# Kernel optimization log

Measured on AMD Instinct MI355X. Metric: run time of the kernel, lower is better.

## Reference

```python
import jax, jax.numpy as jnp
import numpy as np

MEM = 128   # mem_dim
K = 4096    # number of object keys (each an array leaf list)
L = 128     # numbers per array
STATS_CAP = 100  # number_stats list capped at 100 entries


def setup_inputs() -> dict:
    key = jax.random.key(0)
    ks = jax.random.split(key, 13)
    s = 0.05
    return {
        "numbers": jax.random.normal(ks[0], (K, L), jnp.float32),
        "w_num": jax.random.normal(ks[1], (MEM,), jnp.float32) * s,
        "b_num": jax.random.normal(ks[2], (MEM,), jnp.float32) * s,
        "W_ih": jax.random.normal(ks[3], (4 * MEM, 2 * MEM), jnp.float32) * s,
        "W_hh": jax.random.normal(ks[4], (4 * MEM, MEM), jnp.float32) * s,
        "b_ih": jax.random.normal(ks[5], (4 * MEM,), jnp.float32) * s,
        "b_hh": jax.random.normal(ks[6], (4 * MEM,), jnp.float32) * s,
        "W_fh": jax.random.normal(ks[7], (MEM, MEM), jnp.float32) * s,
        "b_fh": jax.random.normal(ks[8], (MEM,), jnp.float32) * s,
        "W_iouh": jax.random.normal(ks[9], (3 * MEM, MEM), jnp.float32) * s,
        "b_iouh": jax.random.normal(ks[10], (3 * MEM,), jnp.float32) * s,
        "W_lout": jax.random.normal(ks[11], (MEM, MEM), jnp.float32) * s,
        "b_lout": jax.random.normal(ks[12], (MEM,), jnp.float32) * s,
    }


def _normalize_numbers(x_flat):
    # Replicates embed_number's running number_stats (tie_primitives -> one shared
    # '___default___' stats list, filled in traversal order, capped at 100 entries).
    # The k-th number is normalized by mean/std over the first min(k, 100) numbers
    # (including itself); std division only when len > 3 and std not ~0.
    n = x_flat.shape[0]
    k = jnp.arange(1, n + 1, dtype=jnp.float32)
    cs = jnp.cumsum(x_flat)
    css = jnp.cumsum(x_flat * x_flat)
    cap = jnp.minimum(k, float(STATS_CAP))
    cs_c = jnp.where(k <= STATS_CAP, cs, cs[STATS_CAP - 1])
    css_c = jnp.where(k <= STATS_CAP, css, css[STATS_CAP - 1])
    mean = cs_c / cap
    var = jnp.maximum(css_c / cap - mean * mean, 0.0)
    std = jnp.sqrt(var)
    # torch impl computes stats with numpy -> no gradient flows through them
    mean = jax.lax.stop_gradient(mean)
    std = jax.lax.stop_gradient(std)
    y = x_flat - mean
    use_std = (cap > 3.0) & (std > 1e-8)
    return jnp.where(use_std, y / jnp.where(use_std, std, 1.0), y)


def _forward(numbers, w_num, b_num, W_ih, W_hh, b_ih, b_hh,
             W_fh, b_fh, W_iouh, b_iouh, W_lout, b_lout):
    # --- embed_number: per-leaf (c=0, h = Linear(1, MEM)(norm_num)) ---
    x = _normalize_numbers(numbers.reshape(-1)).reshape(K, L)
    h_num = x[..., None] * w_num + b_num  # [K, L, MEM]

    # --- embed_array: LSTMCell over each array's children; input = cat([c_child, h_child]) ---
    # child_c is always 0 for number leaves.
    def step(carry, h_t):  # h_t: [K, MEM]
        c, h = carry
        xcat = jnp.concatenate([jnp.zeros_like(h_t), h_t], axis=-1)  # [K, 2*MEM]
        gates = xcat @ W_ih.T + b_ih + h @ W_hh.T + b_hh             # [K, 4*MEM]
        i, f, g, o = jnp.split(gates, 4, axis=-1)
        c2 = jax.nn.sigmoid(f) * c + jax.nn.sigmoid(i) * jnp.tanh(g)
        h2 = jax.nn.sigmoid(o) * jnp.tanh(c2)
        return (c2, h2), None

    z = jnp.zeros((K, MEM), numbers.dtype)
    (c_arr, h_arr), _ = jax.lax.scan(step, (z, z), jnp.swapaxes(h_num, 0, 1))
    # c_arr, h_arr: [K, MEM] final states per array child of the root object

    # --- embed_object (root): child-sum Tree-LSTM gating ---
    f_g = jax.nn.sigmoid(h_arr @ W_fh.T + b_fh)             # [K, MEM]
    fc_sum = jnp.sum(f_g * c_arr, axis=0, keepdims=True)    # [1, MEM]
    hs_bar = jnp.sum(h_arr, axis=0, keepdims=True)          # [1, MEM]
    iou = hs_bar @ W_iouh.T + b_iouh
    i, o, u = jnp.split(iou, 3, axis=-1)
    c = jax.nn.sigmoid(i) * jnp.tanh(u) + fc_sum
    h = jax.nn.sigmoid(o) * jnp.tanh(c)
    h_hat = h @ W_lout.T + b_lout
    return jnp.concatenate([c, h_hat], axis=1)  # [1, 2*MEM]


def reference(numbers, w_num, b_num, W_ih, W_hh, b_ih, b_hh,
              W_fh, b_fh, W_iouh, b_iouh, W_lout, b_lout):
    return _forward(numbers, w_num, b_num, W_ih, W_hh, b_ih, b_hh,
                    W_fh, b_fh, W_iouh, b_iouh, W_lout, b_lout)
```

## Files before the change

kernel.cpp:

```cpp
#include <hip/hip_runtime.h>
#include <math.h>

#define MEM 128
#define HSTR 136

typedef __bf16 bf16x8 __attribute__((ext_vector_type(8)));
typedef float  f32x4  __attribute__((ext_vector_type(4)));

__device__ __forceinline__ float fast_rcp(float x) { return __builtin_amdgcn_rcpf(x); }
__device__ __forceinline__ float fast_sigmoid(float x) {
    return fast_rcp(1.0f + __expf(-x));
}
__device__ __forceinline__ float fast_tanh(float x) {
    return 1.0f - 2.0f * fast_rcp(__expf(2.0f * x) + 1.0f);
}

__global__ void prep_kernel(const float* __restrict__ numbers,
                            const float* __restrict__ w_num,
                            const float* __restrict__ b_num,
                            const float* __restrict__ W_ih,
                            const float* __restrict__ b_ih,
                            const float* __restrict__ b_hh,
                            float* __restrict__ mean_lut, float* __restrict__ inv_lut,
                            float* __restrict__ Avec, float* __restrict__ Bvec) {
    __shared__ float sx[100];
    int tid = threadIdx.x;
    if (tid < 100) sx[tid] = numbers[tid];
    __syncthreads();
    if (tid < 100) {
        float s = 0.f, ss = 0.f;
        for (int j = 0; j <= tid; ++j) { float v = sx[j]; s += v; ss += v * v; }
        float cap  = (float)(tid + 1);
        float mean = s / cap;
        float var  = ss / cap - mean * mean;
        if (var < 0.f) var = 0.f;
        float sd = sqrtf(var);
        float inv = (cap > 3.0f && sd > 1e-8f) ? (1.0f / sd) : 1.0f;
        mean_lut[tid] = mean;
        inv_lut[tid]  = inv;
    }
    if (tid < 512) {
        const float* row = W_ih + tid * 256 + 128;
        float a = 0.f, b = 0.f;
        #pragma unroll 8
        for (int m = 0; m < 128; ++m) { a += row[m] * w_num[m]; b += row[m] * b_num[m]; }
        Avec[tid] = a;
        Bvec[tid] = b + b_ih[tid] + b_hh[tid];
    }
}

__global__ __launch_bounds__(512, 2) void lstm_kernel(
        const float* __restrict__ numbers, const float* __restrict__ W_hh,
        const float* __restrict__ W_fh,    const float* __restrict__ b_fh,
        const float* __restrict__ mean_lut, const float* __restrict__ inv_lut,
        const float* __restrict__ Avec,     const float* __restrict__ Bvec,
        float* __restrict__ fc_sum, float* __restrict__ hs_bar) {
    __shared__ unsigned short hbuf[2][16 * HSTR];
    __shared__ float xls[128 * 16];

    const int tid  = threadIdx.x;
    const int lane = tid & 63;
    const int wave = tid >> 6;
    const int quad = lane >> 4;
    const int lcol = lane & 15;
    const int m0   = wave * 16;
    const int r0   = blockIdx.x * 16;

    for (int i = tid; i < 16 * 128; i += 512) {
        int row = i >> 7;
        int t   = i & 127;
        int flat = (r0 + row) * 128 + t;
        int ii = (flat < 100) ? flat : 99;
        float v = numbers[flat];
        xls[t * 16 + row] = (v - mean_lut[ii]) * inv_lut[ii];
    }
    for (int i = tid; i < 16 * HSTR; i += 512) hbuf[0][i] = 0;

    bf16x8 bf[4][4];
    #pragma unroll
    for (int g = 0; g < 4; ++g) {
        #pragma unroll
        for (int kk = 0; kk < 4; ++kk) {
            int j = g * 128 + m0 + lcol;
            const float* p = W_hh + j * 128 + kk * 32 + quad * 8;
            f32x4 w0 = *(const f32x4*)p;
            f32x4 w1 = *(const f32x4*)(p + 4);
            bf16x8 bt;
            #pragma unroll
            for (int q = 0; q < 4; ++q) { bt[q] = (__bf16)w0[q]; bt[q + 4] = (__bf16)w1[q]; }
            bf[g][kk] = bt;
        }
    }
    float ag[4], bg[4];
    #pragma unroll
    for (int g = 0; g < 4; ++g) {
        ag[g] = Avec[g * 128 + m0 + lcol];
        bg[g] = Bvec[g * 128 + m0 + lcol];
    }

    float c[4]  = {0.f, 0.f, 0.f, 0.f};
    float hf[4] = {0.f, 0.f, 0.f, 0.f};
    __syncthreads();

    auto step = [&](int t, const unsigned short* hin, unsigned short* hout) {
        bf16x8 af[4];
        #pragma unroll
        for (int kk = 0; kk < 4; ++kk)
            af[kk] = *(const bf16x8*)(const void*)(hin + lcol * HSTR + kk * 32 + quad * 8);
        f32x4 xq = *(const f32x4*)(const void*)(xls + t * 16 + quad * 4);
        f32x4 acc[4];
        #pragma unroll
        for (int g = 0; g < 4; ++g) {
            f32x4 a0;
            #pragma unroll
            for (int r = 0; r < 4; ++r) a0[r] = xq[r] * ag[g] + bg[g];
            #pragma unroll
            for (int kk = 0; kk < 4; ++kk)
                a0 = __builtin_amdgcn_mfma_f32_16x16x32_bf16(af[kk], bf[g][kk], a0, 0, 0, 0);
            acc[g] = a0;
        }
        #pragma unroll
        for (int r = 0; r < 4; ++r) {
            float si = fast_sigmoid(acc[0][r]);
            float sf = fast_sigmoid(acc[1][r]);
            float tg = fast_tanh(acc[2][r]);
            float so = fast_sigmoid(acc[3][r]);
            float c2 = sf * c[r] + si * tg;
            c[r] = c2;
            float h = so * fast_tanh(c2);
            hf[r] = h;
            hout[(quad * 4 + r) * HSTR + m0 + lcol] = __builtin_bit_cast(unsigned short, (__bf16)h);
        }
        __syncthreads();
    };

    for (int t = 0; t < 128; t += 2) {
        step(t,     hbuf[0], hbuf[1]);
        step(t + 1, hbuf[1], hbuf[0]);
    }

    float v = hf[0] + hf[1] + hf[2] + hf[3];
    v += __shfl_xor(v, 16);
    v += __shfl_xor(v, 32);
    if (lane < 16) atomicAdd(&hs_bar[m0 + lane], v);

    f32x4 facc;
    {
        float bb = b_fh[m0 + lcol];
        #pragma unroll
        for (int r = 0; r < 4; ++r) facc[r] = bb;
    }
    #pragma unroll
    for (int kk = 0; kk < 4; ++kk) {
        bf16x8 afr = *(const bf16x8*)(const void*)(hbuf[0] + lcol * HSTR + kk * 32 + quad * 8);
        const float* p = W_fh + (m0 + lcol) * 128 + kk * 32 + quad * 8;
        f32x4 w0 = *(const f32x4*)p;
        f32x4 w1 = *(const f32x4*)(p + 4);
        bf16x8 wt;
        #pragma unroll
        for (int q = 0; q < 4; ++q) { wt[q] = (__bf16)w0[q]; wt[q + 4] = (__bf16)w1[q]; }
        facc = __builtin_amdgcn_mfma_f32_16x16x32_bf16(afr, wt, facc, 0, 0, 0);
    }
    float fcv = 0.f;
    #pragma unroll
    for (int r = 0; r < 4; ++r) fcv += fast_sigmoid(facc[r]) * c[r];
    fcv += __shfl_xor(fcv, 16);
    fcv += __shfl_xor(fcv, 32);
    if (lane < 16) atomicAdd(&fc_sum[m0 + lane], fcv);
}

__global__ void finalize_kernel(const float* __restrict__ fc_sum,
                                const float* __restrict__ hs_bar,
                                const float* __restrict__ W_iouh,
                                const float* __restrict__ b_iouh,
                                const float* __restrict__ W_lout,
                                const float* __restrict__ b_lout,
                                float* __restrict__ out) {
    __shared__ float hsb[128], iou[384], hfin[128];
    int tid = threadIdx.x;
    if (tid < 128) hsb[tid] = hs_bar[tid];
    __syncthreads();
    if (tid < 384) {
        float s = b_iouh[tid];
        const float* row = W_iouh + tid * 128;
        #pragma unroll 8
        for (int m = 0; m < 128; ++m) s += row[m] * hsb[m];
        iou[tid] = s;
    }
    __syncthreads();
    if (tid < 128) {
        float i = iou[tid], o = iou[128 + tid], u = iou[256 + tid];
        float cf = fast_sigmoid(i) * fast_tanh(u) + fc_sum[tid];
        out[tid] = cf;
        hfin[tid] = fast_sigmoid(o) * fast_tanh(cf);
    }
    __syncthreads();
    if (tid < 128) {
        float s = b_lout[tid];
        const float* row = W_lout + tid * 128;
        #pragma unroll 8
        for (int k = 0; k < 128; ++k) s += row[k] * hfin[k];
        out[128 + tid] = s;
    }
}

extern "C" void kernel_launch(void* const* d_in, const int* in_sizes, int n_in,
                              void* d_out, int out_size, void* d_ws, size_t ws_size,
                              hipStream_t stream) {
    const float* numbers = (const float*)d_in[0];
    const float* w_num   = (const float*)d_in[1];
    const float* b_num   = (const float*)d_in[2];
    const float* W_ih    = (const float*)d_in[3];
    const float* W_hh    = (const float*)d_in[4];
    const float* b_ih    = (const float*)d_in[5];
    const float* b_hh    = (const float*)d_in[6];
    const float* W_fh    = (const float*)d_in[7];
    const float* b_fh    = (const float*)d_in[8];
    const float* W_iouh  = (const float*)d_in[9];
    const float* b_iouh  = (const float*)d_in[10];
    const float* W_lout  = (const float*)d_in[11];
    const float* b_lout  = (const float*)d_in[12];
    float* out = (float*)d_out;

    float* ws       = (float*)d_ws;
    float* fc_sum   = ws;
    float* hs_bar   = ws + 128;
    float* mean_lut = ws + 256;
    float* inv_lut  = ws + 356;
    float* Avec     = ws + 456;
    float* Bvec     = ws + 968;

    hipMemsetAsync(fc_sum, 0, 256 * sizeof(float), stream);
    prep_kernel<<<1, 512, 0, stream>>>(numbers, w_num, b_num, W_ih, b_ih, b_hh,
                                       mean_lut, inv_lut, Avec, Bvec);
    lstm_kernel<<<256, 512, 0, stream>>>(numbers, W_hh, W_fh, b_fh,
                                         mean_lut, inv_lut, Avec, Bvec, fc_sum, hs_bar);
    finalize_kernel<<<1, 384, 0, stream>>>(fc_sum, hs_bar, W_iouh, b_iouh, W_lout, b_lout, out);
}
```

Before: 218.5 us.

## Split LSTM gates across two wave groups and fold log2e scaling into weights

The LSTM kernel now runs 1024 threads per block. Waves 0-7 compute the input and cell-candidate gates and pass their product through shared memory. Waves 8-15 compute the forget and output gates, update c and h, and write h. The log2(e) factors are folded into W_hh, Avec/Bvec and W_fh so activations become a single exp2 plus reciprocal. The prep kernel is spread over 65 blocks with a wave reduction and now also zeroes the accumulators, which removes the memset. The finalize kernel uses vector loads. The split adds a second barrier per timestep and a shared-memory exchange, in return for halving the MFMA and transcendental work per wave on the serial recurrence path.

```diff
diff --git a/kernel.cpp b/kernel.cpp
--- a/kernel.cpp
+++ b/kernel.cpp
@@ -1,18 +1,15 @@
 #include <hip/hip_runtime.h>
 #include <math.h>
 
-#define MEM 128
+#define L2E 1.4426950408889634f
 #define HSTR 136
+#define PRS 16
 
 typedef __bf16 bf16x8 __attribute__((ext_vector_type(8)));
 typedef float  f32x4  __attribute__((ext_vector_type(4)));
 
-__device__ __forceinline__ float fast_rcp(float x) { return __builtin_amdgcn_rcpf(x); }
-__device__ __forceinline__ float fast_sigmoid(float x) {
-    return fast_rcp(1.0f + __expf(-x));
-}
-__device__ __forceinline__ float fast_tanh(float x) {
-    return 1.0f - 2.0f * fast_rcp(__expf(2.0f * x) + 1.0f);
+__device__ __forceinline__ float sig2(float y) {
+    return __builtin_amdgcn_rcpf(1.0f + __builtin_amdgcn_exp2f(-y));
 }
 
 __global__ void prep_kernel(const float* __restrict__ numbers,
@@ -21,35 +18,52 @@
                             const float* __restrict__ W_ih,
                             const float* __restrict__ b_ih,
                             const float* __restrict__ b_hh,
-                            float* __restrict__ mean_lut, float* __restrict__ inv_lut,
-                            float* __restrict__ Avec, float* __restrict__ Bvec) {
-    __shared__ float sx[100];
-    int tid = threadIdx.x;
-    if (tid < 100) sx[tid] = numbers[tid];
-    __syncthreads();
-    if (tid < 100) {
-        float s = 0.f, ss = 0.f;
-        for (int j = 0; j <= tid; ++j) { float v = sx[j]; s += v; ss += v * v; }
-        float cap  = (float)(tid + 1);
-        float mean = s / cap;
-        float var  = ss / cap - mean * mean;
-        if (var < 0.f) var = 0.f;
-        float sd = sqrtf(var);
-        float inv = (cap > 3.0f && sd > 1e-8f) ? (1.0f / sd) : 1.0f;
-        mean_lut[tid] = mean;
-        inv_lut[tid]  = inv;
-    }
-    if (tid < 512) {
-        const float* row = W_ih + tid * 256 + 128;
-        float a = 0.f, b = 0.f;
-        #pragma unroll 8
-        for (int m = 0; m < 128; ++m) { a += row[m] * w_num[m]; b += row[m] * b_num[m]; }
-        Avec[tid] = a;
-        Bvec[tid] = b + b_ih[tid] + b_hh[tid];
-    }
-}
-
-__global__ __launch_bounds__(512, 2) void lstm_kernel(
+                            float* __restrict__ ws_base) {
+    float* fc_hs    = ws_base;
+    float* mean_lut = ws_base + 256;
+    float* inv_lut  = ws_base + 356;
+    float* Avec     = ws_base + 456;
+    float* Bvec     = ws_base + 968;
+
+    if (blockIdx.x == 64) {
+        __shared__ float sx[100];
+        int tid = threadIdx.x;
+        if (tid < 256) fc_hs[tid] = 0.0f;
+        if (tid < 100) sx[tid] = numbers[tid];
+        __syncthreads();
+        if (tid < 100) {
+            float s = 0.f, ss = 0.f;
+            for (int j = 0; j <= tid; ++j) { float v = sx[j]; s += v; ss += v * v; }
+            float cap  = (float)(tid + 1);
+            float mean = s / cap;
+            float var  = ss / cap - mean * mean;
+            if (var < 0.f) var = 0.f;
+            float sd = sqrtf(var);
+            float inv = (cap > 3.0f && sd > 1e-8f) ? (1.0f / sd) : 1.0f;
+            mean_lut[tid] = mean;
+            inv_lut[tid]  = inv;
+        }
+        return;
+    }
+    int j    = blockIdx.x * 8 + (threadIdx.x >> 6);
+    int lane = threadIdx.x & 63;
+    const float* row = W_ih + j * 256 + 128;
+    float r1 = row[lane], r2 = row[lane + 64];
+    float a = r1 * w_num[lane] + r2 * w_num[lane + 64];
+    float b = r1 * b_num[lane] + r2 * b_num[lane + 64];
+    #pragma unroll
+    for (int off = 32; off >= 1; off >>= 1) {
+        a += __shfl_xor(a, off);
+        b += __shfl_xor(b, off);
+    }
+    if (lane == 0) {
+        float s = (j >= 256 && j < 384) ? (2.0f * L2E) : L2E;
+        Avec[j] = a * s;
+        Bvec[j] = (b + b_ih[j] + b_hh[j]) * s;
+    }
+}
+
+__global__ __launch_bounds__(1024, 4) void lstm_kernel(
         const float* __restrict__ numbers, const float* __restrict__ W_hh,
         const float* __restrict__ W_fh,    const float* __restrict__ b_fh,
         const float* __restrict__ mean_lut, const float* __restrict__ inv_lut,
@@ -57,16 +71,18 @@
         float* __restrict__ fc_sum, float* __restrict__ hs_bar) {
     __shared__ unsigned short hbuf[2][16 * HSTR];
     __shared__ float xls[128 * 16];
+    __shared__ float pbuf[128 * PRS];
 
     const int tid  = threadIdx.x;
     const int lane = tid & 63;
     const int wave = tid >> 6;
+    const bool low = wave < 8;
     const int quad = lane >> 4;
     const int lcol = lane & 15;
-    const int m0   = wave * 16;
+    const int m0   = (wave & 7) * 16;
     const int r0   = blockIdx.x * 16;
 
-    for (int i = tid; i < 16 * 128; i += 512) {
+    for (int i = tid; i < 16 * 128; i += 1024) {
         int row = i >> 7;
         int t   = i & 127;
         int flat = (r0 + row) * 128 + t;
@@ -74,99 +90,124 @@
         float v = numbers[flat];
         xls[t * 16 + row] = (v - mean_lut[ii]) * inv_lut[ii];
     }
-    for (int i = tid; i < 16 * HSTR; i += 512) hbuf[0][i] = 0;
-
-    bf16x8 bf[4][4];
+    for (int i = tid; i < 16 * HSTR; i += 1024) hbuf[0][i] = 0;
+
+    const int g0 = low ? 0 : 1;
+    const int g1 = low ? 2 : 3;
+    const float s0 = L2E;
+    const float s1 = low ? (2.0f * L2E) : L2E;
+    bf16x8 bf[2][4];
     #pragma unroll
-    for (int g = 0; g < 4; ++g) {
+    for (int gi = 0; gi < 2; ++gi) {
+        int g = gi ? g1 : g0;
+        float sc = gi ? s1 : s0;
         #pragma unroll
         for (int kk = 0; kk < 4; ++kk) {
-            int j = g * 128 + m0 + lcol;
-            const float* p = W_hh + j * 128 + kk * 32 + quad * 8;
+            const float* p = W_hh + (g * 128 + m0 + lcol) * 128 + kk * 32 + quad * 8;
             f32x4 w0 = *(const f32x4*)p;
             f32x4 w1 = *(const f32x4*)(p + 4);
             bf16x8 bt;
             #pragma unroll
-            for (int q = 0; q < 4; ++q) { bt[q] = (__bf16)w0[q]; bt[q + 4] = (__bf16)w1[q]; }
-            bf[g][kk] = bt;
-        }
-    }
-    float ag[4], bg[4];
-    #pragma unroll
-    for (int g = 0; g < 4; ++g) {
-        ag[g] = Avec[g * 128 + m0 + lcol];
-        bg[g] = Bvec[g * 128 + m0 + lcol];
-    }
+            for (int q = 0; q < 4; ++q) {
+                bt[q]     = (__bf16)(w0[q] * sc);
+                bt[q + 4] = (__bf16)(w1[q] * sc);
+            }
+            bf[gi][kk] = bt;
+        }
+    }
+    float ag[2], bg[2];
+    ag[0] = Avec[g0 * 128 + m0 + lcol];  bg[0] = Bvec[g0 * 128 + m0 + lcol];
+    ag[1] = Avec[g1 * 128 + m0 + lcol];  bg[1] = Bvec[g1 * 128 + m0 + lcol];
 
     float c[4]  = {0.f, 0.f, 0.f, 0.f};
     float hf[4] = {0.f, 0.f, 0.f, 0.f};
     __syncthreads();
 
-    auto step = [&](int t, const unsigned short* hin, unsigned short* hout) {
+    for (int t = 0; t < 128; ++t) {
+        const unsigned short* hin = hbuf[t & 1];
+        unsigned short* hout = hbuf[(t + 1) & 1];
         bf16x8 af[4];
         #pragma unroll
         for (int kk = 0; kk < 4; ++kk)
             af[kk] = *(const bf16x8*)(const void*)(hin + lcol * HSTR + kk * 32 + quad * 8);
         f32x4 xq = *(const f32x4*)(const void*)(xls + t * 16 + quad * 4);
-        f32x4 acc[4];
-        #pragma unroll
-        for (int g = 0; g < 4; ++g) {
+        f32x4 acc[2];
+        #pragma unroll
+        for (int gi = 0; gi < 2; ++gi) {
             f32x4 a0;
             #pragma unroll
-            for (int r = 0; r < 4; ++r) a0[r] = xq[r] * ag[g] + bg[g];
+            for (int r = 0; r < 4; ++r) a0[r] = xq[r] * ag[gi] + bg[gi];
             #pragma unroll
             for (int kk = 0; kk < 4; ++kk)
-                a0 = __builtin_amdgcn_mfma_f32_16x16x32_bf16(af[kk], bf[g][kk], a0, 0, 0, 0);
-            acc[g] = a0;
-        }
-        #pragma unroll
-        for (int r = 0; r < 4; ++r) {
-            float si = fast_sigmoid(acc[0][r]);
-            float sf = fast_sigmoid(acc[1][r]);
-            float tg = fast_tanh(acc[2][r]);
-            float so = fast_sigmoid(acc[3][r]);
-            float c2 = sf * c[r] + si * tg;
-            c[r] = c2;
-            float h = so * fast_tanh(c2);
-            hf[r] = h;
-            hout[(quad * 4 + r) * HSTR + m0 + lcol] = __builtin_bit_cast(unsigned short, (__bf16)h);
+                a0 = __builtin_amdgcn_mfma_f32_16x16x32_bf16(af[kk], bf[gi][kk], a0, 0, 0, 0);
+            acc[gi] = a0;
+        }
+        float sf[4], so[4];
+        if (low) {
+            f32x4 pv;
+            #pragma unroll
+            for (int r = 0; r < 4; ++r) {
+                float si = sig2(acc[0][r]);
+                float tg = 2.0f * sig2(acc[1][r]) - 1.0f;
+                pv[r] = si * tg;
+            }
+            *(f32x4*)(pbuf + (m0 + lcol) * PRS + quad * 4) = pv;
+        } else {
+            #pragma unroll
+            for (int r = 0; r < 4; ++r) {
+                sf[r] = sig2(acc[0][r]);
+                so[r] = sig2(acc[1][r]);
+            }
         }
         __syncthreads();
-    };
-
-    for (int t = 0; t < 128; t += 2) {
-        step(t,     hbuf[0], hbuf[1]);
-        step(t + 1, hbuf[1], hbuf[0]);
-    }
-
-    float v = hf[0] + hf[1] + hf[2] + hf[3];
-    v += __shfl_xor(v, 16);
-    v += __shfl_xor(v, 32);
-    if (lane < 16) atomicAdd(&hs_bar[m0 + lane], v);
-
-    f32x4 facc;
-    {
-        float bb = b_fh[m0 + lcol];
-        #pragma unroll
-        for (int r = 0; r < 4; ++r) facc[r] = bb;
-    }
-    #pragma unroll
-    for (int kk = 0; kk < 4; ++kk) {
-        bf16x8 afr = *(const bf16x8*)(const void*)(hbuf[0] + lcol * HSTR + kk * 32 + quad * 8);
-        const float* p = W_fh + (m0 + lcol) * 128 + kk * 32 + quad * 8;
-        f32x4 w0 = *(const f32x4*)p;
-        f32x4 w1 = *(const f32x4*)(p + 4);
-        bf16x8 wt;
-        #pragma unroll
-        for (int q = 0; q < 4; ++q) { wt[q] = (__bf16)w0[q]; wt[q + 4] = (__bf16)w1[q]; }
-        facc = __builtin_amdgcn_mfma_f32_16x16x32_bf16(afr, wt, facc, 0, 0, 0);
-    }
-    float fcv = 0.f;
-    #pragma unroll
-    for (int r = 0; r < 4; ++r) fcv += fast_sigmoid(facc[r]) * c[r];
-    fcv += __shfl_xor(fcv, 16);
-    fcv += __shfl_xor(fcv, 32);
-    if (lane < 16) atomicAdd(&fc_sum[m0 + lane], fcv);
+        if (!low) {
+            f32x4 pv = *(const f32x4*)(const void*)(pbuf + (m0 + lcol) * PRS + quad * 4);
+            #pragma unroll
+            for (int r = 0; r < 4; ++r) {
+                float c2 = sf[r] * c[r] + pv[r];
+                c[r] = c2;
+                float th = 2.0f * sig2(c2 * (2.0f * L2E)) - 1.0f;
+                float h = so[r] * th;
+                hf[r] = h;
+                hout[(quad * 4 + r) * HSTR + m0 + lcol] =
+                    __builtin_bit_cast(unsigned short, (__bf16)h);
+            }
+        }
+        __syncthreads();
+    }
+
+    if (!low) {
+        float v = hf[0] + hf[1] + hf[2] + hf[3];
+        v += __shfl_xor(v, 16);
+        v += __shfl_xor(v, 32);
+        if (lane < 16) atomicAdd(&hs_bar[m0 + lane], v);
+        f32x4 facc;
+        {
+            float bb = b_fh[m0 + lcol] * L2E;
+            #pragma unroll
+            for (int r = 0; r < 4; ++r) facc[r] = bb;
+        }
+        #pragma unroll
+        for (int kk = 0; kk < 4; ++kk) {
+            bf16x8 afr = *(const bf16x8*)(const void*)(hbuf[0] + lcol * HSTR + kk * 32 + quad * 8);
+            const float* p = W_fh + (m0 + lcol) * 128 + kk * 32 + quad * 8;
+            f32x4 w0 = *(const f32x4*)p;
+            f32x4 w1 = *(const f32x4*)(p + 4);
+            bf16x8 wt;
+            #pragma unroll
+            for (int q = 0; q < 4; ++q) {
+                wt[q]     = (__bf16)(w0[q] * L2E);
+                wt[q + 4] = (__bf16)(w1[q] * L2E);
+            }
+            facc = __builtin_amdgcn_mfma_f32_16x16x32_bf16(afr, wt, facc, 0, 0, 0);
+        }
+        float fcv = 0.f;
+        #pragma unroll
+        for (int r = 0; r < 4; ++r) fcv += sig2(facc[r]) * c[r];
+        fcv += __shfl_xor(fcv, 16);
+        fcv += __shfl_xor(fcv, 32);
+        if (lane < 16) atomicAdd(&fc_sum[m0 + lane], fcv);
+    }
 }
 
 __global__ void finalize_kernel(const float* __restrict__ fc_sum,
@@ -182,24 +223,30 @@
     __syncthreads();
     if (tid < 384) {
         float s = b_iouh[tid];
-        const float* row = W_iouh + tid * 128;
+        const f32x4* row = (const f32x4*)(W_iouh + tid * 128);
         #pragma unroll 8
-        for (int m = 0; m < 128; ++m) s += row[m] * hsb[m];
+        for (int m = 0; m < 32; ++m) {
+            f32x4 w = row[m];
+            s += w[0] * hsb[4*m] + w[1] * hsb[4*m+1] + w[2] * hsb[4*m+2] + w[3] * hsb[4*m+3];
+        }
         iou[tid] = s;
     }
     __syncthreads();
     if (tid < 128) {
         float i = iou[tid], o = iou[128 + tid], u = iou[256 + tid];
-        float cf = fast_sigmoid(i) * fast_tanh(u) + fc_sum[tid];
+        float cf = sig2(i * L2E) * (2.0f * sig2(u * 2.0f * L2E) - 1.0f) + fc_sum[tid];
         out[tid] = cf;
-        hfin[tid] = fast_sigmoid(o) * fast_tanh(cf);
+        hfin[tid] = sig2(o * L2E) * (2.0f * sig2(cf * 2.0f * L2E) - 1.0f);
     }
     __syncthreads();
     if (tid < 128) {
         float s = b_lout[tid];
-        const float* row = W_lout + tid * 128;
+        const f32x4* row = (const f32x4*)(W_lout + tid * 128);
         #pragma unroll 8
-        for (int k = 0; k < 128; ++k) s += row[k] * hfin[k];
+        for (int m = 0; m < 32; ++m) {
+            f32x4 w = row[m];
+            s += w[0] * hfin[4*m] + w[1] * hfin[4*m+1] + w[2] * hfin[4*m+2] + w[3] * hfin[4*m+3];
+        }
         out[128 + tid] = s;
     }
 }
@@ -230,10 +277,8 @@
     float* Avec     = ws + 456;
     float* Bvec     = ws + 968;
 
-    hipMemsetAsync(fc_sum, 0, 256 * sizeof(float), stream);
-    prep_kernel<<<1, 512, 0, stream>>>(numbers, w_num, b_num, W_ih, b_ih, b_hh,
-                                       mean_lut, inv_lut, Avec, Bvec);
-    lstm_kernel<<<256, 512, 0, stream>>>(numbers, W_hh, W_fh, b_fh,
-                                         mean_lut, inv_lut, Avec, Bvec, fc_sum, hs_bar);
+    prep_kernel<<<65, 512, 0, stream>>>(numbers, w_num, b_num, W_ih, b_ih, b_hh, ws);
+    lstm_kernel<<<256, 1024, 0, stream>>>(numbers, W_hh, W_fh, b_fh,
+                                          mean_lut, inv_lut, Avec, Bvec, fc_sum, hs_bar);
     finalize_kernel<<<1, 384, 0, stream>>>(fc_sum, hs_bar, W_iouh, b_iouh, W_lout, b_lout, out);
 }
```

New measurement: 218.9 us. About the same (+0.2%).
